# Kernel tuning notes

Hardware: AMD Instinct MI355X
Metric: run time of the kernel (lower is better)

The kernel has to match this reference:

```python
import jax, jax.numpy as jnp
import numpy as np

BETA = 0.0  # vcon_steps=0 -> beta=0 -> pure MAM (max+min); beta=1 would be standard GEMM


def setup_inputs() -> dict:
    key = jax.random.key(0)
    k1, k2, k3 = jax.random.split(key, 3)
    in_features, out_features = 512, 512
    x = jax.random.normal(k1, (8, 128, in_features), dtype=jnp.float32)
    # kaiming_uniform-ish scale for weight, uniform bound for bias
    bound_w = float(np.sqrt(1.0 / in_features))
    weight = jax.random.uniform(k2, (out_features, in_features), dtype=jnp.float32,
                                minval=-bound_w, maxval=bound_w)
    bias = jax.random.uniform(k3, (out_features,), dtype=jnp.float32,
                              minval=-bound_w, maxval=bound_w)
    return {"x": x, "weight": weight, "bias": bias}


def reference(x, weight, bias):
    # x: [..., K]; weight: [M, K]; bias: [M]
    K = x.shape[-1]
    xf = x.reshape(-1, K)                      # [N, K]
    # elementwise products per (row, input, output): [N, K, M]
    P = xf[:, :, None] * weight.T[None, :, :]
    pmax = jnp.max(P, axis=1)                  # [N, M]
    argmax = jnp.argmax(P, axis=1).astype(jnp.int32)
    pmin = jnp.min(P, axis=1)                  # [N, M]
    argmin = jnp.argmin(P, axis=1).astype(jnp.int32)
    mam = pmax + pmin
    if BETA > 0.0:
        full = jnp.einsum('nk,mk->nm', xf, weight)
        C_flat = mam + BETA * (full - mam) + bias
    else:
        C_flat = mam + bias
    C = C_flat.reshape(x.shape[:-1] + (weight.shape[0],))
    return C, argmax, argmin
```

## Files before the change

kernel.cpp:

```cpp
#include <hip/hip_runtime.h>
#include <math.h>


constexpr int NTOT = 1024;
constexpr int MTOT = 512;
constexpr int KTOT = 512;
constexpr int BN = 32;
constexpr int BM = 32;
constexpr int BK = 128;
constexpr int G  = 16;
constexpr int LDSP = BK + 4;

__device__ __forceinline__ float max3f(float a, float b, float c) {
  float d; asm("v_max3_f32 %0, %1, %2, %3" : "=v"(d) : "v"(a), "v"(b), "v"(c)); return d;
}
__device__ __forceinline__ float min3f(float a, float b, float c) {
  float d; asm("v_min3_f32 %0, %1, %2, %3" : "=v"(d) : "v"(a), "v"(b), "v"(c)); return d;
}
__device__ __forceinline__ float fmul0(float a, float b) {
  float d; asm("v_fma_f32 %0, %1, %2, 0" : "=v"(d) : "v"(a), "v"(b)); return d;
}
__device__ __forceinline__ float4 f4mul(float4 a, float4 b) {
  return make_float4(fmul0(a.x, b.x), fmul0(a.y, b.y), fmul0(a.z, b.z), fmul0(a.w, b.w));
}

#define CELL(S, A0, A1, A2, A3, B0, B1, B2, B3)                              \
  {                                                                          \
    const float4 q0 = f4mul(A0, B0), q1 = f4mul(A1, B1);                     \
    const float4 q2 = f4mul(A2, B2), q3 = f4mul(A3, B3);                     \
    const float M = fmaxf(max3f(max3f(q0.x, q0.y, q0.z),                     \
                                max3f(q0.w, q1.x, q1.y),                     \
                                max3f(q1.z, q1.w, q2.x)),                    \
                          max3f(max3f(q2.y, q2.z, q2.w), q3.x,               \
                                max3f(q3.y, q3.z, q3.w)));                   \
    const float m = fminf(min3f(min3f(q0.x, q0.y, q0.z),                     \
                                min3f(q0.w, q1.x, q1.y),                     \
                                min3f(q1.z, q1.w, q2.x)),                    \
                          min3f(min3f(q2.y, q2.z, q2.w), q3.x,               \
                                min3f(q3.y, q3.z, q3.w)));                   \
    const bool u = M > vmax##S;                                              \
    vmax##S = u ? M : vmax##S;  gx##S = u ? gk : gx##S;                      \
    const bool v = m < vmin##S;                                              \
    vmin##S = v ? m : vmin##S;  gn##S = v ? gk : gn##S;                      \
  }

#define MERGE(S, RR, CC)                                                     \
  {                                                                          \
    const int cell = (RR) * 32 + (CC);                                       \
    const float pmx = comb[cell * 4 + 0];                                    \
    const int   pgx = __float_as_int(comb[cell * 4 + 1]);                    \
    const float pmn = comb[cell * 4 + 2];                                    \
    const int   pgn = __float_as_int(comb[cell * 4 + 3]);                    \
    if (pmx > vmax##S) { vmax##S = pmx; gx##S = pgx; }                       \
    else if (pmx == vmax##S && pgx < gx##S) { gx##S = pgx; }                 \
    if (pmn < vmin##S) { vmin##S = pmn; gn##S = pgn; }                       \
    else if (pmn == vmin##S && pgn < gn##S) { gn##S = pgn; }                 \
  }

__device__ __forceinline__ int find_first_eq(const float* __restrict__ xr,
                                             const float* __restrict__ wr,
                                             float tgt, int base) {
  const float4 a0 = *(const float4*)(xr + 0),  a1 = *(const float4*)(xr + 4);
  const float4 a2 = *(const float4*)(xr + 8),  a3 = *(const float4*)(xr + 12);
  const float4 b0 = *(const float4*)(wr + 0),  b1 = *(const float4*)(wr + 4);
  const float4 b2 = *(const float4*)(wr + 8),  b3 = *(const float4*)(wr + 12);
  int idx = base;
  idx = (a3.w * b3.w == tgt) ? base + 15 : idx;
  idx = (a3.z * b3.z == tgt) ? base + 14 : idx;
  idx = (a3.y * b3.y == tgt) ? base + 13 : idx;
  idx = (a3.x * b3.x == tgt) ? base + 12 : idx;
  idx = (a2.w * b2.w == tgt) ? base + 11 : idx;
  idx = (a2.z * b2.z == tgt) ? base + 10 : idx;
  idx = (a2.y * b2.y == tgt) ? base +  9 : idx;
  idx = (a2.x * b2.x == tgt) ? base +  8 : idx;
  idx = (a1.w * b1.w == tgt) ? base +  7 : idx;
  idx = (a1.z * b1.z == tgt) ? base +  6 : idx;
  idx = (a1.y * b1.y == tgt) ? base +  5 : idx;
  idx = (a1.x * b1.x == tgt) ? base +  4 : idx;
  idx = (a0.w * b0.w == tgt) ? base +  3 : idx;
  idx = (a0.z * b0.z == tgt) ? base +  2 : idx;
  idx = (a0.y * b0.y == tgt) ? base +  1 : idx;
  idx = (a0.x * b0.x == tgt) ? base +  0 : idx;
  return idx;
}

__global__ __launch_bounds__(512, 4) void mam_kernel(
    const float* __restrict__ X,
    const float* __restrict__ W,
    const float* __restrict__ B,
    float* __restrict__ out)
{
  __shared__ float sx[BN][LDSP];
  __shared__ float sw[BM][LDSP];

  const int th   = threadIdx.x;
  const int half = th >> 8;
  const int t    = th & 255;
  const int n0 = blockIdx.y * BN;
  const int m0 = blockIdx.x * BM;

  const int tn = t >> 4;
  const int tm = t & 15;
  const int r0 = tn, r1 = tn + 16;
  const int c0 = tm, c1 = tm + 16;
  const int kbase = half * 64;

  float vmax00 = -INFINITY, vmax01 = -INFINITY, vmax10 = -INFINITY, vmax11 = -INFINITY;
  float vmin00 =  INFINITY, vmin01 =  INFINITY, vmin10 =  INFINITY, vmin11 =  INFINITY;
  int   gx00 = 0, gx01 = 0, gx10 = 0, gx11 = 0;
  int   gn00 = 0, gn01 = 0, gn10 = 0, gn11 = 0;

  #pragma unroll 1
  for (int kc = 0; kc < KTOT; kc += BK) {
    __syncthreads();
    #pragma unroll
    for (int j = 0; j < 2; ++j) {
      const int id = th + 512 * j;
      const int r  = id >> 5;
      const int f  = id & 31;
      *reinterpret_cast<float4*>(&sx[r][f * 4]) =
          *reinterpret_cast<const float4*>(&X[(n0 + r) * KTOT + kc + f * 4]);
      *reinterpret_cast<float4*>(&sw[r][f * 4]) =
          *reinterpret_cast<const float4*>(&W[(m0 + r) * KTOT + kc + f * 4]);
    }
    __syncthreads();

    #pragma unroll
    for (int g8 = 0; g8 < 4; ++g8) {
      const int off = kbase + g8 * G;
      const int gk  = kc + off;
      const float4* xap = reinterpret_cast<const float4*>(&sx[r0][off]);
      const float4* xbp = reinterpret_cast<const float4*>(&sx[r1][off]);
      const float4* wap = reinterpret_cast<const float4*>(&sw[c0][off]);
      const float4* wbp = reinterpret_cast<const float4*>(&sw[c1][off]);
      const float4 xa0 = xap[0], xa1 = xap[1], xa2 = xap[2], xa3 = xap[3];
      const float4 xb0 = xbp[0], xb1 = xbp[1], xb2 = xbp[2], xb3 = xbp[3];
      const float4 wa0 = wap[0], wa1 = wap[1], wa2 = wap[2], wa3 = wap[3];
      const float4 wb0 = wbp[0], wb1 = wbp[1], wb2 = wbp[2], wb3 = wbp[3];

      CELL(00, xa0, xa1, xa2, xa3, wa0, wa1, wa2, wa3)
      CELL(01, xa0, xa1, xa2, xa3, wb0, wb1, wb2, wb3)
      CELL(10, xb0, xb1, xb2, xb3, wa0, wa1, wa2, wa3)
      CELL(11, xb0, xb1, xb2, xb3, wb0, wb1, wb2, wb3)
    }
  }

  __syncthreads();
  float* comb = &sx[0][0];
  if (half == 1) {
    const int cells[4][2] = {{r0, c0}, {r0, c1}, {r1, c0}, {r1, c1}};
    const float vals[4][2] = {{vmax00, vmin00}, {vmax01, vmin01},
                              {vmax10, vmin10}, {vmax11, vmin11}};
    const int gids[4][2] = {{gx00, gn00}, {gx01, gn01}, {gx10, gn10}, {gx11, gn11}};
    #pragma unroll
    for (int i = 0; i < 4; ++i) {
      const int cell = cells[i][0] * 32 + cells[i][1];
      comb[cell * 4 + 0] = vals[i][0];
      comb[cell * 4 + 1] = __int_as_float(gids[i][0]);
      comb[cell * 4 + 2] = vals[i][1];
      comb[cell * 4 + 3] = __int_as_float(gids[i][1]);
    }
  }
  __syncthreads();

  if (half == 0) {
    MERGE(00, r0, c0)
    MERGE(01, r0, c1)
    MERGE(10, r1, c0)
    MERGE(11, r1, c1)

    const float* Xr0 = &X[(n0 + r0) * KTOT];
    const float* Xr1 = &X[(n0 + r1) * KTOT];
    const float* Wc0 = &W[(m0 + c0) * KTOT];
    const float* Wc1 = &W[(m0 + c1) * KTOT];

    const int imax00 = find_first_eq(Xr0 + gx00, Wc0 + gx00, vmax00, gx00);
    const int imin00 = find_first_eq(Xr0 + gn00, Wc0 + gn00, vmin00, gn00);
    const int imax01 = find_first_eq(Xr0 + gx01, Wc1 + gx01, vmax01, gx01);
    const int imin01 = find_first_eq(Xr0 + gn01, Wc1 + gn01, vmin01, gn01);
    const int imax10 = find_first_eq(Xr1 + gx10, Wc0 + gx10, vmax10, gx10);
    const int imin10 = find_first_eq(Xr1 + gn10, Wc0 + gn10, vmin10, gn10);
    const int imax11 = find_first_eq(Xr1 + gx11, Wc1 + gx11, vmax11, gx11);
    const int imin11 = find_first_eq(Xr1 + gn11, Wc1 + gn11, vmin11, gn11);

    float* Cout = out;
    float* AM   = out + NTOT * MTOT;
    float* AN   = AM + NTOT * MTOT;

    const float b0 = B[m0 + c0];
    const float b1 = B[m0 + c1];

    const int o00 = (n0 + r0) * MTOT + (m0 + c0);
    const int o01 = (n0 + r0) * MTOT + (m0 + c1);
    const int o10 = (n0 + r1) * MTOT + (m0 + c0);
    const int o11 = (n0 + r1) * MTOT + (m0 + c1);

    Cout[o00] = vmax00 + vmin00 + b0;  AM[o00] = (float)imax00;  AN[o00] = (float)imin00;
    Cout[o01] = vmax01 + vmin01 + b1;  AM[o01] = (float)imax01;  AN[o01] = (float)imin01;
    Cout[o10] = vmax10 + vmin10 + b0;  AM[o10] = (float)imax10;  AN[o10] = (float)imin10;
    Cout[o11] = vmax11 + vmin11 + b1;  AM[o11] = (float)imax11;  AN[o11] = (float)imin11;
  }
}

extern "C" void kernel_launch(void* const* d_in, const int* in_sizes, int n_in,
                              void* d_out, int out_size, void* d_ws, size_t ws_size,
                              hipStream_t stream) {
  const float* X = (const float*)d_in[0];
  const float* W = (const float*)d_in[1];
  const float* B = (const float*)d_in[2];
  float* out = (float*)d_out;

  dim3 grid(MTOT / BM, NTOT / BN);
  mam_kernel<<<grid, dim3(512), 0, stream>>>(X, W, B, out);
}
```

Before: 32.61 us.

## Load X directly from global memory instead of staging through LDS

Removes the shared-memory tile for X. Each thread now reads its two X rows straight from global memory as float4 vectors, while W is still staged in LDS. This cuts LDS capacity and store traffic, which may allow more resident blocks. The cost is redundant global or L1/L2 reads of X across the 16 threads sharing a row, and longer latency in the inner loop. The merge-buffer writes and reads also become single float4 accesses instead of four scalar ones.

```diff
diff --git a/kernel.cpp b/kernel.cpp
--- a/kernel.cpp
+++ b/kernel.cpp
@@ -9,7 +9,7 @@
 constexpr int BM = 32;
 constexpr int BK = 128;
 constexpr int G  = 16;
-constexpr int LDSP = BK + 4;
+constexpr int LDSP = 132;
 
 __device__ __forceinline__ float max3f(float a, float b, float c) {
   float d; asm("v_max3_f32 %0, %1, %2, %3" : "=v"(d) : "v"(a), "v"(b), "v"(c)); return d;
@@ -22,39 +22,29 @@
 }
 __device__ __forceinline__ float4 f4mul(float4 a, float4 b) {
   return make_float4(fmul0(a.x, b.x), fmul0(a.y, b.y), fmul0(a.z, b.z), fmul0(a.w, b.w));
+}
+
+__device__ __forceinline__ void tree16(const float4& q0, const float4& q1,
+                                       const float4& q2, const float4& q3,
+                                       float& M, float& m) {
+  M = fmaxf(max3f(max3f(q0.x, q0.y, q0.z), max3f(q0.w, q1.x, q1.y),
+                  max3f(q1.z, q1.w, q2.x)),
+            max3f(max3f(q2.y, q2.z, q2.w), q3.x, max3f(q3.y, q3.z, q3.w)));
+  m = fminf(min3f(min3f(q0.x, q0.y, q0.z), min3f(q0.w, q1.x, q1.y),
+                  min3f(q1.z, q1.w, q2.x)),
+            min3f(min3f(q2.y, q2.z, q2.w), q3.x, min3f(q3.y, q3.z, q3.w)));
 }
 
 #define CELL(S, A0, A1, A2, A3, B0, B1, B2, B3)                              \
   {                                                                          \
     const float4 q0 = f4mul(A0, B0), q1 = f4mul(A1, B1);                     \
     const float4 q2 = f4mul(A2, B2), q3 = f4mul(A3, B3);                     \
-    const float M = fmaxf(max3f(max3f(q0.x, q0.y, q0.z),                     \
-                                max3f(q0.w, q1.x, q1.y),                     \
-                                max3f(q1.z, q1.w, q2.x)),                    \
-                          max3f(max3f(q2.y, q2.z, q2.w), q3.x,               \
-                                max3f(q3.y, q3.z, q3.w)));                   \
-    const float m = fminf(min3f(min3f(q0.x, q0.y, q0.z),                     \
-                                min3f(q0.w, q1.x, q1.y),                     \
-                                min3f(q1.z, q1.w, q2.x)),                    \
-                          min3f(min3f(q2.y, q2.z, q2.w), q3.x,               \
-                                min3f(q3.y, q3.z, q3.w)));                   \
+    float M, m;                                                              \
+    tree16(q0, q1, q2, q3, M, m);                                            \
     const bool u = M > vmax##S;                                              \
     vmax##S = u ? M : vmax##S;  gx##S = u ? gk : gx##S;                      \
     const bool v = m < vmin##S;                                              \
     vmin##S = v ? m : vmin##S;  gn##S = v ? gk : gn##S;                      \
-  }
-
-#define MERGE(S, RR, CC)                                                     \
-  {                                                                          \
-    const int cell = (RR) * 32 + (CC);                                       \
-    const float pmx = comb[cell * 4 + 0];                                    \
-    const int   pgx = __float_as_int(comb[cell * 4 + 1]);                    \
-    const float pmn = comb[cell * 4 + 2];                                    \
-    const int   pgn = __float_as_int(comb[cell * 4 + 3]);                    \
-    if (pmx > vmax##S) { vmax##S = pmx; gx##S = pgx; }                       \
-    else if (pmx == vmax##S && pgx < gx##S) { gx##S = pgx; }                 \
-    if (pmn < vmin##S) { vmin##S = pmn; gn##S = pgn; }                       \
-    else if (pmn == vmin##S && pgn < gn##S) { gn##S = pgn; }                 \
   }
 
 __device__ __forceinline__ int find_first_eq(const float* __restrict__ xr,
@@ -90,7 +80,6 @@
     const float* __restrict__ B,
     float* __restrict__ out)
 {
-  __shared__ float sx[BN][LDSP];
   __shared__ float sw[BM][LDSP];
 
   const int th   = threadIdx.x;
@@ -104,6 +93,9 @@
   const int r0 = tn, r1 = tn + 16;
   const int c0 = tm, c1 = tm + 16;
   const int kbase = half * 64;
+
+  const float* Xr0 = &X[(n0 + r0) * KTOT];
+  const float* Xr1 = &X[(n0 + r1) * KTOT];
 
   float vmax00 = -INFINITY, vmax01 = -INFINITY, vmax10 = -INFINITY, vmax11 = -INFINITY;
   float vmin00 =  INFINITY, vmin01 =  INFINITY, vmin10 =  INFINITY, vmin11 =  INFINITY;
@@ -118,23 +110,25 @@
       const int id = th + 512 * j;
       const int r  = id >> 5;
       const int f  = id & 31;
-      *reinterpret_cast<float4*>(&sx[r][f * 4]) =
-          *reinterpret_cast<const float4*>(&X[(n0 + r) * KTOT + kc + f * 4]);
       *reinterpret_cast<float4*>(&sw[r][f * 4]) =
           *reinterpret_cast<const float4*>(&W[(m0 + r) * KTOT + kc + f * 4]);
     }
     __syncthreads();
 
     #pragma unroll
-    for (int g8 = 0; g8 < 4; ++g8) {
-      const int off = kbase + g8 * G;
+    for (int g = 0; g < 4; ++g) {
+      const int off = kbase + g * G;
       const int gk  = kc + off;
-      const float4* xap = reinterpret_cast<const float4*>(&sx[r0][off]);
-      const float4* xbp = reinterpret_cast<const float4*>(&sx[r1][off]);
+      const float4 xa0 = *reinterpret_cast<const float4*>(Xr0 + gk + 0);
+      const float4 xa1 = *reinterpret_cast<const float4*>(Xr0 + gk + 4);
+      const float4 xa2 = *reinterpret_cast<const float4*>(Xr0 + gk + 8);
+      const float4 xa3 = *reinterpret_cast<const float4*>(Xr0 + gk + 12);
+      const float4 xb0 = *reinterpret_cast<const float4*>(Xr1 + gk + 0);
+      const float4 xb1 = *reinterpret_cast<const float4*>(Xr1 + gk + 4);
+      const float4 xb2 = *reinterpret_cast<const float4*>(Xr1 + gk + 8);
+      const float4 xb3 = *reinterpret_cast<const float4*>(Xr1 + gk + 12);
       const float4* wap = reinterpret_cast<const float4*>(&sw[c0][off]);
       const float4* wbp = reinterpret_cast<const float4*>(&sw[c1][off]);
-      const float4 xa0 = xap[0], xa1 = xap[1], xa2 = xap[2], xa3 = xap[3];
-      const float4 xb0 = xbp[0], xb1 = xbp[1], xb2 = xbp[2], xb3 = xbp[3];
       const float4 wa0 = wap[0], wa1 = wap[1], wa2 = wap[2], wa3 = wap[3];
       const float4 wb0 = wbp[0], wb1 = wbp[1], wb2 = wbp[2], wb3 = wbp[3];
 
@@ -146,7 +140,7 @@
   }
 
   __syncthreads();
-  float* comb = &sx[0][0];
+  float* comb = &sw[0][0];
   if (half == 1) {
     const int cells[4][2] = {{r0, c0}, {r0, c1}, {r1, c0}, {r1, c1}};
     const float vals[4][2] = {{vmax00, vmin00}, {vmax01, vmin01},
@@ -155,22 +149,29 @@
     #pragma unroll
     for (int i = 0; i < 4; ++i) {
       const int cell = cells[i][0] * 32 + cells[i][1];
-      comb[cell * 4 + 0] = vals[i][0];
-      comb[cell * 4 + 1] = __int_as_float(gids[i][0]);
-      comb[cell * 4 + 2] = vals[i][1];
-      comb[cell * 4 + 3] = __int_as_float(gids[i][1]);
+      *reinterpret_cast<float4*>(&comb[cell * 4]) =
+          make_float4(vals[i][0], __int_as_float(gids[i][0]),
+                      vals[i][1], __int_as_float(gids[i][1]));
     }
   }
   __syncthreads();
 
   if (half == 0) {
+#define MERGE(S, RR, CC)                                                     \
+    {                                                                        \
+      const float4 v_ = *reinterpret_cast<const float4*>(&comb[((RR) * 32 + (CC)) * 4]); \
+      const float pmx = v_.x;  const int pgx = __float_as_int(v_.y);         \
+      const float pmn = v_.z;  const int pgn = __float_as_int(v_.w);         \
+      if (pmx > vmax##S) { vmax##S = pmx; gx##S = pgx; }                     \
+      else if (pmx == vmax##S && pgx < gx##S) { gx##S = pgx; }               \
+      if (pmn < vmin##S) { vmin##S = pmn; gn##S = pgn; }                     \
+      else if (pmn == vmin##S && pgn < gn##S) { gn##S = pgn; }               \
+    }
     MERGE(00, r0, c0)
     MERGE(01, r0, c1)
     MERGE(10, r1, c0)
     MERGE(11, r1, c1)
 
-    const float* Xr0 = &X[(n0 + r0) * KTOT];
-    const float* Xr1 = &X[(n0 + r1) * KTOT];
     const float* Wc0 = &W[(m0 + c0) * KTOT];
     const float* Wc1 = &W[(m0 + c1) * KTOT];
 
```

Result: slower. 34.76 us (+6.6%).
